# Optimization experiments

Hardware: AMD Instinct MI355X
Metric: run time of the kernel (lower is better)

## Reference

```python
import jax, jax.numpy as jnp
import numpy as np

B, IN, OUT = 2048, 64, 2048


def setup_inputs() -> dict:
    key = jax.random.key(0)
    k1, k2, k3 = jax.random.split(key, 3)
    x = jax.random.normal(k1, (B, IN), dtype=jnp.float32)
    # learned params (shapes per init: means [in, out], inv_std_dev [out, in, in])
    means = jax.random.uniform(k2, (IN, OUT), dtype=jnp.float32)
    # roughly like the inverse of a diagonal step matrix plus small noise
    inv_std_dev = (jax.random.normal(k3, (OUT, IN, IN), dtype=jnp.float32) * 0.05
                   + jnp.eye(IN, dtype=jnp.float32) * 0.5)
    return {"x": x, "means": means, "inv_std_dev": inv_std_dev}


def reference(x, means, inv_std_dev):
    # diff[b, o, i] = x[b, i] - means[i, o]   -> [B, OUT, IN]
    d = x[:, None, :] - means.T[None, :, :]
    # torch uses inv_std_dev.pow(2) (elementwise square), not a matrix square
    A = inv_std_dev * inv_std_dev  # [OUT, IN, IN]
    # per-neuron quadratic form: q[b, o] = d[b,o,:] @ A[o] @ d[b,o,:]
    q = jnp.einsum('boi,oij,boj->bo', d, A, d)
    return jnp.exp(-0.5 * q)  # [B, OUT]
```

## Files before the change

### kernel.cpp

```cpp
#include <hip/hip_runtime.h>
#include <hip/hip_bf16.h>

typedef __bf16 bf16x8 __attribute__((ext_vector_type(8)));
typedef float f32x4 __attribute__((ext_vector_type(4)));
typedef float f32x16 __attribute__((ext_vector_type(16)));

#define B_N 2048
#define O_N 2048
#define K_N 64

__device__ __forceinline__ void gld16(const void* g, void* l) {
    __builtin_amdgcn_global_load_lds(
        (const __attribute__((address_space(1))) void*)g,
        (__attribute__((address_space(3))) void*)l,
        16, 0, 0);
}

__global__ __launch_bounds__(256) void rbf_prep(
    const float* __restrict__ inv, const float* __restrict__ means,
    __bf16* __restrict__ Atp, __bf16* __restrict__ cPhi,
    __bf16* __restrict__ cPlo, float* __restrict__ kArr)
{
    __shared__ float s[64 * 65];
    __shared__ float mld[64];
    __shared__ float uw[128];
    const int o = blockIdx.x;
    const int t = threadIdx.x;
    const float4* src = (const float4*)(inv + (size_t)o * 4096);
#pragma unroll
    for (int k = 0; k < 4; ++k) {
        const int idx = k * 256 + t;
        const float4 v = src[idx];
        const int i = idx >> 4;
        const int j0 = (idx & 15) * 4;
        s[i * 65 + j0 + 0] = v.x * v.x;
        s[i * 65 + j0 + 1] = v.y * v.y;
        s[i * 65 + j0 + 2] = v.z * v.z;
        s[i * 65 + j0 + 3] = v.w * v.w;
    }
    if (t < 64) mld[t] = means[(size_t)t * O_N + o];
    __syncthreads();
    if (t < 64) {
        float u = 0.f;
#pragma unroll
        for (int i = 0; i < 64; ++i) u = fmaf(s[i * 65 + t], mld[i], u);
        uw[t] = u;
    } else if (t < 128) {
        const int j = t - 64;
        float w = 0.f;
#pragma unroll
        for (int i = 0; i < 64; ++i) w = fmaf(s[j * 65 + i], mld[i], w);
        uw[64 + j] = w;
    }
    __syncthreads();
    if (t < 64) {
        const float c = -(uw[t] + uw[64 + t]);
        const __bf16 hi = (__bf16)c;
        const __bf16 lo = (__bf16)(c - (float)hi);
        const size_t eidx = (size_t)(o >> 5) * 2048 + (size_t)(t >> 4) * 512
                          + (size_t)(o & 31) * 16 + (t & 15);
        cPhi[eidx] = hi;
        cPlo[eidx] = lo;
    }
    if (t == 0) {
        float kk = 0.f;
#pragma unroll
        for (int j = 0; j < 64; ++j) kk = fmaf(uw[j], mld[j], kk);
        kArr[o] = kk;
    }
#pragma unroll
    for (int r = 0; r < 2; ++r) {
        const int ch = r * 256 + t;
        const int ss = ch >> 7;
        const int j = (ch >> 1) & 63;
        const int hh = ch & 1;
        bf16x8 v;
#pragma unroll
        for (int e = 0; e < 8; ++e)
            v[e] = (__bf16)s[(16 * ss + 8 * hh + e) * 65 + j];
        *(bf16x8*)(Atp + (size_t)o * 4096 + (size_t)ch * 8) = v;
    }
}

__global__ __launch_bounds__(256, 4) void rbf_main(
    const float* __restrict__ x, const __bf16* __restrict__ Atp,
    const __bf16* __restrict__ cPhi, const __bf16* __restrict__ cPlo,
    const float* __restrict__ kArr, float* __restrict__ out)
{
    __shared__ __align__(16) __bf16 sA[2][4096];
    __shared__ __align__(16) float sLin[4][32][32];
    __shared__ float sK[32];

    const int tid = threadIdx.x;
    const int wave = tid >> 6;
    const int lane = tid & 63;
    const int b = lane & 31;
    const int h = lane >> 5;

    const int wg = (int)blockIdx.x;
    const int xcd = wg & 7;
    const int loc = wg >> 3;
    const int og = xcd * 8 + (loc >> 4);
    const int bg = loc & 15;
    const int oBase = og * 32;
    const int rowW = bg * 128 + wave * 32;

    const float* xr = x + (size_t)(rowW + b) * K_N;

    const f32x16 zz = {0.f,0.f,0.f,0.f,0.f,0.f,0.f,0.f,
                       0.f,0.f,0.f,0.f,0.f,0.f,0.f,0.f};

    bf16x8 xh[4];
    f32x4 xd[2][4];
    {
        bf16x8 xl[4];
#pragma unroll
        for (int ss = 0; ss < 4; ++ss) {
            const float* p = xr + ss * 16 + h * 8;
            bf16x8 vh, vl;
#pragma unroll
            for (int e = 0; e < 8; ++e) {
                const float v = p[e];
                const __bf16 hi = (__bf16)v;
                vh[e] = hi;
                vl[e] = (__bf16)(v - (float)hi);
            }
            xh[ss] = vh; xl[ss] = vl;
        }
#pragma unroll
        for (int mt = 0; mt < 2; ++mt)
#pragma unroll
            for (int rq = 0; rq < 4; ++rq)
                xd[mt][rq] = *(const f32x4*)(xr + mt * 32 + rq * 8 + h * 4);

        const __bf16* chp = cPhi + (size_t)og * 2048;
        const __bf16* clp = cPlo + (size_t)og * 2048;
        f32x16 lin = zz;
#pragma unroll
        for (int ss = 0; ss < 4; ++ss) {
            const bf16x8 fh = *(const bf16x8*)(chp + ss * 512 + b * 16 + h * 8);
            const bf16x8 fl = *(const bf16x8*)(clp + ss * 512 + b * 16 + h * 8);
            lin = __builtin_amdgcn_mfma_f32_32x32x16_bf16(fh, xh[ss], lin, 0, 0, 0);
            lin = __builtin_amdgcn_mfma_f32_32x32x16_bf16(fh, xl[ss], lin, 0, 0, 0);
            lin = __builtin_amdgcn_mfma_f32_32x32x16_bf16(fl, xh[ss], lin, 0, 0, 0);
        }
#pragma unroll
        for (int r = 0; r < 16; ++r)
            sLin[wave][(r & 3) + 8 * (r >> 2) + 4 * h][b] = lin[r];
    }
    if (tid < 32) sK[tid] = kArr[oBase + tid];

    const int L0 = tid * 16, L1 = 4096 + tid * 16;
    const int S0 = L0 ^ (((L0 >> 7) & 7) << 4);
    const int S1 = L1 ^ (((L1 >> 7) & 7) << 4);
    const char* gp = (const char*)(Atp + (size_t)oBase * 4096);
    gld16(gp + S0, (char*)&sA[0][0] + L0);
    gld16(gp + S1, (char*)&sA[0][0] + L1);

    const int off0 = (b * 32 + h * 16) ^ (((b >> 2) & 7) << 4);
    float* outp = out + (size_t)(rowW + b) * O_N + oBase;

    float q4[4];
#pragma unroll 4
    for (int i = 0; i < 32; ++i) {
        __syncthreads();
        if (i < 31) {
            const char* gn = gp + (size_t)(i + 1) * 8192;
            char* ld = (char*)&sA[(i + 1) & 1][0];
            gld16(gn + S0, ld + L0);
            gld16(gn + S1, ld + L1);
        }
        const char* bufp = (const char*)&sA[i & 1][0];

        __builtin_amdgcn_s_setprio(1);
        f32x16 a0 = zz, a1 = zz;
#pragma unroll
        for (int ss = 0; ss < 4; ++ss) {
            const char* base = bufp + ss * 2048;
            const bf16x8 f0 = *(const bf16x8*)(base + off0);
            const bf16x8 f1 = *(const bf16x8*)(base + 1024 + off0);
            a0 = __builtin_amdgcn_mfma_f32_32x32x16_bf16(f0, xh[ss], a0, 0, 0, 0);
            a1 = __builtin_amdgcn_mfma_f32_32x32x16_bf16(f1, xh[ss], a1, 0, 0, 0);
        }
        __builtin_amdgcn_s_setprio(0);

        float p0 = 0.f, p1 = 0.f, p2 = 0.f, p3 = 0.f;
#pragma unroll
        for (int e = 0; e < 4; ++e) {
            p0 = fmaf(a0[e],      xd[0][0][e], p0);
            p1 = fmaf(a0[4 + e],  xd[0][1][e], p1);
            p2 = fmaf(a0[8 + e],  xd[0][2][e], p2);
            p3 = fmaf(a0[12 + e], xd[0][3][e], p3);
            p0 = fmaf(a1[e],      xd[1][0][e], p0);
            p1 = fmaf(a1[4 + e],  xd[1][1][e], p1);
            p2 = fmaf(a1[8 + e],  xd[1][2][e], p2);
            p3 = fmaf(a1[12 + e], xd[1][3][e], p3);
        }
        float q = (p0 + p1) + (p2 + p3);
        q += __shfl_xor(q, 32, 64);
        q += sLin[wave][i][b] + sK[i];
        q4[i & 3] = exp2f(q * -0.72134752044448170368f);

        if ((i & 3) == 3 && h == ((i >> 2) & 1)) {
            const f32x4 v = {q4[0], q4[1], q4[2], q4[3]};
            *(f32x4*)(outp + (i - 3)) = v;
        }
    }
}

extern "C" void kernel_launch(void* const* d_in, const int* in_sizes, int n_in,
                              void* d_out, int out_size, void* d_ws, size_t ws_size,
                              hipStream_t stream)
{
    const float* x = (const float*)d_in[0];
    const float* means = (const float*)d_in[1];
    const float* inv = (const float*)d_in[2];
    float* out = (float*)d_out;

    char* w = (char*)d_ws;
    __bf16* Atp  = (__bf16*)w;
    __bf16* cPhi = (__bf16*)(w + (size_t)O_N * 4096 * 2);
    __bf16* cPlo = (__bf16*)(w + (size_t)O_N * 4096 * 2 + 262144);
    float*  kArr = (float*)(w + (size_t)O_N * 4096 * 2 + 524288);

    rbf_prep<<<dim3(O_N), dim3(256), 0, stream>>>(inv, means, Atp, cPhi, cPlo, kArr);
    rbf_main<<<dim3(1024), dim3(256), 0, stream>>>(x, Atp, cPhi, cPlo, kArr, out);

    (void)in_sizes; (void)n_in; (void)out_size; (void)ws_size;
}
```

Measured before the change: 63.65 us.

## Quad-buffer A tiles, halve barriers, keep linear term in registers

The main loop now uses four LDS buffers and loads two A tiles per barrier, so there is one __syncthreads for every two output neurons instead of one per neuron. The linear term plus constant is kept in registers, with kArr added into the MFMA result, rather than being staged through the sLin/sK shared arrays. The loop is fully unrolled through macros, the first MFMA starts from zero instead of a zeroed accumulator, and the final dot uses packed two-wide FMAs. The exp is computed only in the half-wave that stores. LDS use goes from about 16.5KB to 32KB per block, which could limit occupancy under launch_bounds(256,4), and code size grows.

```diff
diff --git a/kernel.cpp b/kernel.cpp
--- a/kernel.cpp
+++ b/kernel.cpp
@@ -2,6 +2,7 @@
 #include <hip/hip_bf16.h>
 
 typedef __bf16 bf16x8 __attribute__((ext_vector_type(8)));
+typedef float f32x2 __attribute__((ext_vector_type(2)));
 typedef float f32x4 __attribute__((ext_vector_type(4)));
 typedef float f32x16 __attribute__((ext_vector_type(16)));
 
@@ -87,9 +88,7 @@
     const __bf16* __restrict__ cPhi, const __bf16* __restrict__ cPlo,
     const float* __restrict__ kArr, float* __restrict__ out)
 {
-    __shared__ __align__(16) __bf16 sA[2][4096];
-    __shared__ __align__(16) float sLin[4][32][32];
-    __shared__ float sK[32];
+    __shared__ __align__(16) __bf16 sA[4][4096];
 
     const int tid = threadIdx.x;
     const int wave = tid >> 6;
@@ -112,6 +111,7 @@
 
     bf16x8 xh[4];
     f32x4 xd[2][4];
+    f32x16 lin;
     {
         bf16x8 xl[4];
 #pragma unroll
@@ -135,7 +135,7 @@
 
         const __bf16* chp = cPhi + (size_t)og * 2048;
         const __bf16* clp = cPlo + (size_t)og * 2048;
-        f32x16 lin = zz;
+        lin = zz;
 #pragma unroll
         for (int ss = 0; ss < 4; ++ss) {
             const bf16x8 fh = *(const bf16x8*)(chp + ss * 512 + b * 16 + h * 8);
@@ -146,9 +146,8 @@
         }
 #pragma unroll
         for (int r = 0; r < 16; ++r)
-            sLin[wave][(r & 3) + 8 * (r >> 2) + 4 * h][b] = lin[r];
-    }
-    if (tid < 32) sK[tid] = kArr[oBase + tid];
+            lin[r] += kArr[oBase + (r & 3) + 8 * (r >> 2) + 4 * h];
+    }
 
     const int L0 = tid * 16, L1 = 4096 + tid * 16;
     const int S0 = L0 ^ (((L0 >> 7) & 7) << 4);
@@ -156,56 +155,85 @@
     const char* gp = (const char*)(Atp + (size_t)oBase * 4096);
     gld16(gp + S0, (char*)&sA[0][0] + L0);
     gld16(gp + S1, (char*)&sA[0][0] + L1);
+    gld16(gp + 8192 + S0, (char*)&sA[1][0] + L0);
+    gld16(gp + 8192 + S1, (char*)&sA[1][0] + L1);
 
     const int off0 = (b * 32 + h * 16) ^ (((b >> 2) & 7) << 4);
     float* outp = out + (size_t)(rowW + b) * O_N + oBase;
-
     float q4[4];
-#pragma unroll 4
-    for (int i = 0; i < 32; ++i) {
-        __syncthreads();
-        if (i < 31) {
-            const char* gn = gp + (size_t)(i + 1) * 8192;
-            char* ld = (char*)&sA[(i + 1) & 1][0];
-            gld16(gn + S0, ld + L0);
-            gld16(gn + S1, ld + L1);
-        }
-        const char* bufp = (const char*)&sA[i & 1][0];
-
-        __builtin_amdgcn_s_setprio(1);
-        f32x16 a0 = zz, a1 = zz;
-#pragma unroll
-        for (int ss = 0; ss < 4; ++ss) {
-            const char* base = bufp + ss * 2048;
-            const bf16x8 f0 = *(const bf16x8*)(base + off0);
-            const bf16x8 f1 = *(const bf16x8*)(base + 1024 + off0);
-            a0 = __builtin_amdgcn_mfma_f32_32x32x16_bf16(f0, xh[ss], a0, 0, 0, 0);
-            a1 = __builtin_amdgcn_mfma_f32_32x32x16_bf16(f1, xh[ss], a1, 0, 0, 0);
-        }
-        __builtin_amdgcn_s_setprio(0);
-
-        float p0 = 0.f, p1 = 0.f, p2 = 0.f, p3 = 0.f;
-#pragma unroll
-        for (int e = 0; e < 4; ++e) {
-            p0 = fmaf(a0[e],      xd[0][0][e], p0);
-            p1 = fmaf(a0[4 + e],  xd[0][1][e], p1);
-            p2 = fmaf(a0[8 + e],  xd[0][2][e], p2);
-            p3 = fmaf(a0[12 + e], xd[0][3][e], p3);
-            p0 = fmaf(a1[e],      xd[1][0][e], p0);
-            p1 = fmaf(a1[4 + e],  xd[1][1][e], p1);
-            p2 = fmaf(a1[8 + e],  xd[1][2][e], p2);
-            p3 = fmaf(a1[12 + e], xd[1][3][e], p3);
-        }
-        float q = (p0 + p1) + (p2 + p3);
-        q += __shfl_xor(q, 32, 64);
-        q += sLin[wave][i][b] + sK[i];
-        q4[i & 3] = exp2f(q * -0.72134752044448170368f);
-
-        if ((i & 3) == 3 && h == ((i >> 2) & 1)) {
-            const f32x4 v = {q4[0], q4[1], q4[2], q4[3]};
-            *(f32x4*)(outp + (i - 3)) = v;
-        }
-    }
+
+#define RBF_COMPUTE(I) do {                                                   \
+    const char* bufp_ = (const char*)&sA[(I) & 3][0];                         \
+    __builtin_amdgcn_s_setprio(1);                                            \
+    f32x16 a0_, a1_;                                                          \
+    {                                                                         \
+        const bf16x8 f0_ = *(const bf16x8*)(bufp_ + off0);                    \
+        const bf16x8 f1_ = *(const bf16x8*)(bufp_ + 1024 + off0);             \
+        a0_ = __builtin_amdgcn_mfma_f32_32x32x16_bf16(f0_, xh[0], zz, 0, 0, 0); \
+        a1_ = __builtin_amdgcn_mfma_f32_32x32x16_bf16(f1_, xh[0], zz, 0, 0, 0); \
+    }                                                                         \
+    _Pragma("unroll")                                                         \
+    for (int ss = 1; ss < 4; ++ss) {                                          \
+        const char* base_ = bufp_ + ss * 2048;                                \
+        const bf16x8 f0_ = *(const bf16x8*)(base_ + off0);                    \
+        const bf16x8 f1_ = *(const bf16x8*)(base_ + 1024 + off0);             \
+        a0_ = __builtin_amdgcn_mfma_f32_32x32x16_bf16(f0_, xh[ss], a0_, 0, 0, 0); \
+        a1_ = __builtin_amdgcn_mfma_f32_32x32x16_bf16(f1_, xh[ss], a1_, 0, 0, 0); \
+    }                                                                         \
+    __builtin_amdgcn_s_setprio(0);                                            \
+    f32x2 P0_ = {0.f, 0.f}, P1_ = {0.f, 0.f};                                 \
+    _Pragma("unroll")                                                         \
+    for (int rg = 0; rg < 4; ++rg) {                                          \
+        f32x2 u_, v_;                                                         \
+        u_[0] = a0_[rg*4+0]; u_[1] = a0_[rg*4+1];                             \
+        v_[0] = xd[0][rg][0]; v_[1] = xd[0][rg][1];                           \
+        P0_ = __builtin_elementwise_fma(u_, v_, P0_);                         \
+        u_[0] = a0_[rg*4+2]; u_[1] = a0_[rg*4+3];                             \
+        v_[0] = xd[0][rg][2]; v_[1] = xd[0][rg][3];                           \
+        P1_ = __builtin_elementwise_fma(u_, v_, P1_);                         \
+        u_[0] = a1_[rg*4+0]; u_[1] = a1_[rg*4+1];                             \
+        v_[0] = xd[1][rg][0]; v_[1] = xd[1][rg][1];                           \
+        P0_ = __builtin_elementwise_fma(u_, v_, P0_);                         \
+        u_[0] = a1_[rg*4+2]; u_[1] = a1_[rg*4+3];                             \
+        v_[0] = xd[1][rg][2]; v_[1] = xd[1][rg][3];                           \
+        P1_ = __builtin_elementwise_fma(u_, v_, P1_);                         \
+    }                                                                         \
+    const f32x2 Ps_ = P0_ + P1_;                                              \
+    float q_ = Ps_[0] + Ps_[1];                                               \
+    q_ += __shfl_xor(q_, 32, 64);                                             \
+    if (h == (((I) >> 2) & 1)) {                                              \
+        q4[(I) & 3] = exp2f((q_ + lin[((I) & 3) + (((I) >> 3) << 2)])         \
+                            * -0.72134752044448170368f);                      \
+        if (((I) & 3) == 3) {                                                 \
+            const f32x4 v_ = {q4[0], q4[1], q4[2], q4[3]};                    \
+            *(f32x4*)(outp + ((I) - 3)) = v_;                                 \
+        }                                                                     \
+    }                                                                         \
+} while (0)
+
+#define RBF_PHASE(P) do {                                                     \
+    __syncthreads();                                                          \
+    if ((P) < 15) {                                                           \
+        const char* g2_ = gp + (size_t)(2 * (P) + 2) * 8192;                  \
+        char* d2_ = (char*)&sA[(2 * (P) + 2) & 3][0];                         \
+        gld16(g2_ + S0, d2_ + L0);                                            \
+        gld16(g2_ + S1, d2_ + L1);                                            \
+        const char* g3_ = gp + (size_t)(2 * (P) + 3) * 8192;                  \
+        char* d3_ = (char*)&sA[(2 * (P) + 3) & 3][0];                         \
+        gld16(g3_ + S0, d3_ + L0);                                            \
+        gld16(g3_ + S1, d3_ + L1);                                            \
+    }                                                                         \
+    RBF_COMPUTE(2 * (P));                                                     \
+    RBF_COMPUTE(2 * (P) + 1);                                                 \
+} while (0)
+
+    RBF_PHASE(0);  RBF_PHASE(1);  RBF_PHASE(2);  RBF_PHASE(3);
+    RBF_PHASE(4);  RBF_PHASE(5);  RBF_PHASE(6);  RBF_PHASE(7);
+    RBF_PHASE(8);  RBF_PHASE(9);  RBF_PHASE(10); RBF_PHASE(11);
+    RBF_PHASE(12); RBF_PHASE(13); RBF_PHASE(14); RBF_PHASE(15);
+
+#undef RBF_PHASE
+#undef RBF_COMPUTE
 }
 
 extern "C" void kernel_launch(void* const* d_in, const int* in_sizes, int n_in,
```

After: 60.65 us. 4.7% less time.

## Recast per-neuron quadratic form as single GEMM over symmetric quadratic features

Applied to the files above, without the earlier changes.

Each quadratic form is expanded into upper-triangle monomial features x_i*x_j (2080 terms) plus linear and constant terms. Symmetrised A coefficients, the linear coefficients (split hi/lo) and the constant are packed into one K=2304 bf16 row per output, and matching feature rows per batch element. One plain 64x64-tiled bf16 MFMA GEMM plus an exp epilogue then replaces the per-output matrix-vector products and the FMA reductions. This trades a larger K (2304 against roughly 64x64 per output) for a regular GEMM, and adds preprocessing that writes about 18 MB of workspace. Accuracy may suffer because the x_i*x_j products and symmetrised coefficients are rounded to bf16 with no hi/lo split.

```diff
diff --git a/kernel.cpp b/kernel.cpp
--- a/kernel.cpp
+++ b/kernel.cpp
@@ -2,12 +2,13 @@
 #include <hip/hip_bf16.h>
 
 typedef __bf16 bf16x8 __attribute__((ext_vector_type(8)));
-typedef float f32x4 __attribute__((ext_vector_type(4)));
 typedef float f32x16 __attribute__((ext_vector_type(16)));
 
 #define B_N 2048
 #define O_N 2048
-#define K_N 64
+#define K_TRI 2080
+#define K_TOT 2304
+#define K_STEPS 36
 
 __device__ __forceinline__ void gld16(const void* g, void* l) {
     __builtin_amdgcn_global_load_lds(
@@ -16,195 +17,187 @@
         16, 0, 0);
 }
 
-__global__ __launch_bounds__(256) void rbf_prep(
+__global__ __launch_bounds__(256) void rbf_prep2(
     const float* __restrict__ inv, const float* __restrict__ means,
-    __bf16* __restrict__ Atp, __bf16* __restrict__ cPhi,
-    __bf16* __restrict__ cPlo, float* __restrict__ kArr)
+    const float* __restrict__ x, __bf16* __restrict__ S, __bf16* __restrict__ P)
 {
     __shared__ float s[64 * 65];
     __shared__ float mld[64];
     __shared__ float uw[128];
-    const int o = blockIdx.x;
+    __shared__ unsigned short ptab[K_TRI];
+
     const int t = threadIdx.x;
-    const float4* src = (const float4*)(inv + (size_t)o * 4096);
-#pragma unroll
-    for (int k = 0; k < 4; ++k) {
-        const int idx = k * 256 + t;
-        const float4 v = src[idx];
-        const int i = idx >> 4;
-        const int j0 = (idx & 15) * 4;
-        s[i * 65 + j0 + 0] = v.x * v.x;
-        s[i * 65 + j0 + 1] = v.y * v.y;
-        s[i * 65 + j0 + 2] = v.z * v.z;
-        s[i * 65 + j0 + 3] = v.w * v.w;
-    }
-    if (t < 64) mld[t] = means[(size_t)t * O_N + o];
-    __syncthreads();
-    if (t < 64) {
-        float u = 0.f;
-#pragma unroll
-        for (int i = 0; i < 64; ++i) u = fmaf(s[i * 65 + t], mld[i], u);
-        uw[t] = u;
-    } else if (t < 128) {
-        const int j = t - 64;
-        float w = 0.f;
-#pragma unroll
-        for (int i = 0; i < 64; ++i) w = fmaf(s[j * 65 + i], mld[i], w);
-        uw[64 + j] = w;
-    }
-    __syncthreads();
-    if (t < 64) {
-        const float c = -(uw[t] + uw[64 + t]);
-        const __bf16 hi = (__bf16)c;
-        const __bf16 lo = (__bf16)(c - (float)hi);
-        const size_t eidx = (size_t)(o >> 5) * 2048 + (size_t)(t >> 4) * 512
-                          + (size_t)(o & 31) * 16 + (t & 15);
-        cPhi[eidx] = hi;
-        cPlo[eidx] = lo;
-    }
-    if (t == 0) {
-        float kk = 0.f;
-#pragma unroll
-        for (int j = 0; j < 64; ++j) kk = fmaf(uw[j], mld[j], kk);
-        kArr[o] = kk;
-    }
-#pragma unroll
-    for (int r = 0; r < 2; ++r) {
-        const int ch = r * 256 + t;
-        const int ss = ch >> 7;
-        const int j = (ch >> 1) & 63;
-        const int hh = ch & 1;
-        bf16x8 v;
-#pragma unroll
-        for (int e = 0; e < 8; ++e)
-            v[e] = (__bf16)s[(16 * ss + 8 * hh + e) * 65 + j];
-        *(bf16x8*)(Atp + (size_t)o * 4096 + (size_t)ch * 8) = v;
-    }
-}
-
-__global__ __launch_bounds__(256, 4) void rbf_main(
-    const float* __restrict__ x, const __bf16* __restrict__ Atp,
-    const __bf16* __restrict__ cPhi, const __bf16* __restrict__ cPlo,
-    const float* __restrict__ kArr, float* __restrict__ out)
+    {
+        int base = 0;
+#pragma unroll 1
+        for (int i = 0; i < 64; ++i) {
+            if (t < 64 - i) ptab[base + t] = (unsigned short)((i << 8) | (i + t));
+            base += 64 - i;
+        }
+    }
+
+    if ((int)blockIdx.x < O_N) {
+        const int o = blockIdx.x;
+        const float4* src = (const float4*)(inv + (size_t)o * 4096);
+#pragma unroll
+        for (int k = 0; k < 4; ++k) {
+            const int idx = k * 256 + t;
+            const float4 v = src[idx];
+            const int i = idx >> 4;
+            const int j0 = (idx & 15) * 4;
+            s[i * 65 + j0 + 0] = v.x * v.x;
+            s[i * 65 + j0 + 1] = v.y * v.y;
+            s[i * 65 + j0 + 2] = v.z * v.z;
+            s[i * 65 + j0 + 3] = v.w * v.w;
+        }
+        if (t < 64) mld[t] = means[(size_t)t * O_N + o];
+        __syncthreads();
+        if (t < 64) {
+            float u = 0.f;
+#pragma unroll
+            for (int i = 0; i < 64; ++i) u = fmaf(s[i * 65 + t], mld[i], u);
+            uw[t] = u;
+        } else if (t < 128) {
+            const int j = t - 64;
+            float w = 0.f;
+#pragma unroll
+            for (int i = 0; i < 64; ++i) w = fmaf(s[j * 65 + i], mld[i], w);
+            uw[64 + j] = w;
+        }
+        __syncthreads();
+        __bf16* Srow = S + (size_t)o * K_TOT;
+#pragma unroll 1
+        for (int p = t; p < K_TRI; p += 256) {
+            const int ij = ptab[p];
+            const int i = ij >> 8, j = ij & 255;
+            const float v = (i == j) ? s[i * 65 + i]
+                                     : (s[i * 65 + j] + s[j * 65 + i]);
+            Srow[p] = (__bf16)v;
+        }
+        if (t < 64) {
+            const float c = -(uw[t] + uw[64 + t]);
+            const __bf16 hi = (__bf16)c;
+            const __bf16 lo = (__bf16)(c - (float)hi);
+            Srow[K_TRI + t] = hi;
+            Srow[K_TRI + 64 + t] = hi;
+            Srow[K_TRI + 128 + t] = lo;
+        }
+        if (t == 0) {
+            float kk = 0.f;
+#pragma unroll
+            for (int j = 0; j < 64; ++j) kk = fmaf(uw[j], mld[j], kk);
+            const __bf16 khi = (__bf16)kk;
+            const __bf16 klo = (__bf16)(kk - (float)khi);
+            Srow[2272] = khi;
+            Srow[2273] = klo;
+        }
+        if (t < K_TOT - 2274) Srow[2274 + t] = (__bf16)0.f;
+    } else {
+        const int b = (int)blockIdx.x - O_N;
+        if (t < 64) mld[t] = x[(size_t)b * 64 + t];
+        __syncthreads();
+        __bf16* Prow = P + (size_t)b * K_TOT;
+#pragma unroll 1
+        for (int p = t; p < K_TRI; p += 256) {
+            const int ij = ptab[p];
+            Prow[p] = (__bf16)(mld[ij >> 8] * mld[ij & 255]);
+        }
+        if (t < 64) {
+            const float v = mld[t];
+            const __bf16 hi = (__bf16)v;
+            Prow[K_TRI + t] = hi;
+            Prow[K_TRI + 64 + t] = (__bf16)(v - (float)hi);
+            Prow[K_TRI + 128 + t] = hi;
+        }
+        if (t == 0) {
+            Prow[2272] = (__bf16)1.f;
+            Prow[2273] = (__bf16)1.f;
+        }
+        if (t < K_TOT - 2274) Prow[2274 + t] = (__bf16)0.f;
+    }
+}
+
+__global__ __launch_bounds__(256, 4) void rbf_gemm(
+    const __bf16* __restrict__ P, const __bf16* __restrict__ S,
+    float* __restrict__ out)
 {
-    __shared__ __align__(16) __bf16 sA[2][4096];
-    __shared__ __align__(16) float sLin[4][32][32];
-    __shared__ float sK[32];
+    __shared__ __align__(16) char sP[2][8192];
+    __shared__ __align__(16) char sS[2][8192];
 
     const int tid = threadIdx.x;
-    const int wave = tid >> 6;
     const int lane = tid & 63;
-    const int b = lane & 31;
+    const int w = tid >> 6;
+    const int wr = w >> 1, wc = w & 1;
+    const int cl = lane & 31;
     const int h = lane >> 5;
 
     const int wg = (int)blockIdx.x;
     const int xcd = wg & 7;
     const int loc = wg >> 3;
-    const int og = xcd * 8 + (loc >> 4);
-    const int bg = loc & 15;
-    const int oBase = og * 32;
-    const int rowW = bg * 128 + wave * 32;
-
-    const float* xr = x + (size_t)(rowW + b) * K_N;
+    const int ogl = loc & 3;
+    const int bg = loc >> 2;
+    const int oBase = (xcd * 4 + ogl) * 64;
+    const int bBase = bg * 64;
+
+    const int L0 = tid * 16, L1 = 4096 + tid * 16;
+    const int r0 = L0 >> 7, r1 = L1 >> 7;
+    const int c0 = (L0 & 127) ^ ((r0 & 7) << 4);
+    const int c1 = (L1 & 127) ^ ((r1 & 7) << 4);
+    const char* gP0 = (const char*)P + (size_t)(bBase + r0) * (K_TOT * 2) + c0;
+    const char* gP1 = (const char*)P + (size_t)(bBase + r1) * (K_TOT * 2) + c1;
+    const char* gS0 = (const char*)S + (size_t)(oBase + r0) * (K_TOT * 2) + c0;
+    const char* gS1 = (const char*)S + (size_t)(oBase + r1) * (K_TOT * 2) + c1;
+
+    const int arow = wr * 32 + cl;
+    const int brow = wc * 32 + cl;
+    const char* aPb = &sP[0][0] + arow * 128;
+    const char* aSb = &sS[0][0] + brow * 128;
+    const int mA = (arow & 7) << 4;
+    const int mB = (brow & 7) << 4;
+
+    gld16(gP0, &sP[0][0] + L0);
+    gld16(gP1, &sP[0][0] + L1);
+    gld16(gS0, &sS[0][0] + L0);
+    gld16(gS1, &sS[0][0] + L1);
 
     const f32x16 zz = {0.f,0.f,0.f,0.f,0.f,0.f,0.f,0.f,
                        0.f,0.f,0.f,0.f,0.f,0.f,0.f,0.f};
-
-    bf16x8 xh[4];
-    f32x4 xd[2][4];
-    {
-        bf16x8 xl[4];
-#pragma unroll
-        for (int ss = 0; ss < 4; ++ss) {
-            const float* p = xr + ss * 16 + h * 8;
-            bf16x8 vh, vl;
-#pragma unroll
-            for (int e = 0; e < 8; ++e) {
-                const float v = p[e];
-                const __bf16 hi = (__bf16)v;
-                vh[e] = hi;
-                vl[e] = (__bf16)(v - (float)hi);
-            }
-            xh[ss] = vh; xl[ss] = vl;
-        }
-#pragma unroll
-        for (int mt = 0; mt < 2; ++mt)
-#pragma unroll
-            for (int rq = 0; rq < 4; ++rq)
-                xd[mt][rq] = *(const f32x4*)(xr + mt * 32 + rq * 8 + h * 4);
-
-        const __bf16* chp = cPhi + (size_t)og * 2048;
-        const __bf16* clp = cPlo + (size_t)og * 2048;
-        f32x16 lin = zz;
-#pragma unroll
-        for (int ss = 0; ss < 4; ++ss) {
-            const bf16x8 fh = *(const bf16x8*)(chp + ss * 512 + b * 16 + h * 8);
-            const bf16x8 fl = *(const bf16x8*)(clp + ss * 512 + b * 16 + h * 8);
-            lin = __builtin_amdgcn_mfma_f32_32x32x16_bf16(fh, xh[ss], lin, 0, 0, 0);
-            lin = __builtin_amdgcn_mfma_f32_32x32x16_bf16(fh, xl[ss], lin, 0, 0, 0);
-            lin = __builtin_amdgcn_mfma_f32_32x32x16_bf16(fl, xh[ss], lin, 0, 0, 0);
-        }
-#pragma unroll
-        for (int r = 0; r < 16; ++r)
-            sLin[wave][(r & 3) + 8 * (r >> 2) + 4 * h][b] = lin[r];
-    }
-    if (tid < 32) sK[tid] = kArr[oBase + tid];
-
-    const int L0 = tid * 16, L1 = 4096 + tid * 16;
-    const int S0 = L0 ^ (((L0 >> 7) & 7) << 4);
-    const int S1 = L1 ^ (((L1 >> 7) & 7) << 4);
-    const char* gp = (const char*)(Atp + (size_t)oBase * 4096);
-    gld16(gp + S0, (char*)&sA[0][0] + L0);
-    gld16(gp + S1, (char*)&sA[0][0] + L1);
-
-    const int off0 = (b * 32 + h * 16) ^ (((b >> 2) & 7) << 4);
-    float* outp = out + (size_t)(rowW + b) * O_N + oBase;
-
-    float q4[4];
-#pragma unroll 4
-    for (int i = 0; i < 32; ++i) {
-        __syncthreads();
-        if (i < 31) {
-            const char* gn = gp + (size_t)(i + 1) * 8192;
-            char* ld = (char*)&sA[(i + 1) & 1][0];
-            gld16(gn + S0, ld + L0);
-            gld16(gn + S1, ld + L1);
-        }
-        const char* bufp = (const char*)&sA[i & 1][0];
-
+    f32x16 acc0 = zz, acc1 = zz;
+
+#pragma unroll 2
+    for (int st = 0; st < K_STEPS; ++st) {
+        __syncthreads();
+        if (st < K_STEPS - 1) {
+            const int nb = (st + 1) & 1;
+            const size_t go = (size_t)(st + 1) * 128;
+            gld16(gP0 + go, &sP[nb][0] + L0);
+            gld16(gP1 + go, &sP[nb][0] + L1);
+            gld16(gS0 + go, &sS[nb][0] + L0);
+            gld16(gS1 + go, &sS[nb][0] + L1);
+        }
+        const int bo = (st & 1) * 8192;
+        const bf16x8 a0 = *(const bf16x8*)(aPb + bo + ((0  + h * 16) ^ mA));
+        const bf16x8 b0 = *(const bf16x8*)(aSb + bo + ((0  + h * 16) ^ mB));
+        const bf16x8 a1 = *(const bf16x8*)(aPb + bo + ((32 + h * 16) ^ mA));
+        const bf16x8 b1 = *(const bf16x8*)(aSb + bo + ((32 + h * 16) ^ mB));
+        const bf16x8 a2 = *(const bf16x8*)(aPb + bo + ((64 + h * 16) ^ mA));
+        const bf16x8 b2 = *(const bf16x8*)(aSb + bo + ((64 + h * 16) ^ mB));
+        const bf16x8 a3 = *(const bf16x8*)(aPb + bo + ((96 + h * 16) ^ mA));
+        const bf16x8 b3 = *(const bf16x8*)(aSb + bo + ((96 + h * 16) ^ mB));
         __builtin_amdgcn_s_setprio(1);
-        f32x16 a0 = zz, a1 = zz;
-#pragma unroll
-        for (int ss = 0; ss < 4; ++ss) {
-            const char* base = bufp + ss * 2048;
-            const bf16x8 f0 = *(const bf16x8*)(base + off0);
-            const bf16x8 f1 = *(const bf16x8*)(base + 1024 + off0);
-            a0 = __builtin_amdgcn_mfma_f32_32x32x16_bf16(f0, xh[ss], a0, 0, 0, 0);
-            a1 = __builtin_amdgcn_mfma_f32_32x32x16_bf16(f1, xh[ss], a1, 0, 0, 0);
-        }
+        acc0 = __builtin_amdgcn_mfma_f32_32x32x16_bf16(a0, b0, acc0, 0, 0, 0);
+        acc1 = __builtin_amdgcn_mfma_f32_32x32x16_bf16(a1, b1, acc1, 0, 0, 0);
+        acc0 = __builtin_amdgcn_mfma_f32_32x32x16_bf16(a2, b2, acc0, 0, 0, 0);
+        acc1 = __builtin_amdgcn_mfma_f32_32x32x16_bf16(a3, b3, acc1, 0, 0, 0);
         __builtin_amdgcn_s_setprio(0);
-
-        float p0 = 0.f, p1 = 0.f, p2 = 0.f, p3 = 0.f;
-#pragma unroll
-        for (int e = 0; e < 4; ++e) {
-            p0 = fmaf(a0[e],      xd[0][0][e], p0);
-            p1 = fmaf(a0[4 + e],  xd[0][1][e], p1);
-            p2 = fmaf(a0[8 + e],  xd[0][2][e], p2);
-            p3 = fmaf(a0[12 + e], xd[0][3][e], p3);
-            p0 = fmaf(a1[e],      xd[1][0][e], p0);
-            p1 = fmaf(a1[4 + e],  xd[1][1][e], p1);
-            p2 = fmaf(a1[8 + e],  xd[1][2][e], p2);
-            p3 = fmaf(a1[12 + e], xd[1][3][e], p3);
-        }
-        float q = (p0 + p1) + (p2 + p3);
-        q += __shfl_xor(q, 32, 64);
-        q += sLin[wave][i][b] + sK[i];
-        q4[i & 3] = exp2f(q * -0.72134752044448170368f);
-
-        if ((i & 3) == 3 && h == ((i >> 2) & 1)) {
-            const f32x4 v = {q4[0], q4[1], q4[2], q4[3]};
-            *(f32x4*)(outp + (i - 3)) = v;
-        }
+    }
+
+    const f32x16 accv = acc0 + acc1;
+#pragma unroll
+    for (int r = 0; r < 16; ++r) {
+        const int row = (r & 3) + 8 * (r >> 2) + 4 * h;
+        out[(size_t)(bBase + wr * 32 + row) * O_N + oBase + wc * 32 + cl] =
+            exp2f(accv[r] * -0.72134752044448170368f);
     }
 }
 
@@ -217,14 +210,11 @@
     const float* inv = (const float*)d_in[2];
     float* out = (float*)d_out;
 
-    char* w = (char*)d_ws;
-    __bf16* Atp  = (__bf16*)w;
-    __bf16* cPhi = (__bf16*)(w + (size_t)O_N * 4096 * 2);
-    __bf16* cPlo = (__bf16*)(w + (size_t)O_N * 4096 * 2 + 262144);
-    float*  kArr = (float*)(w + (size_t)O_N * 4096 * 2 + 524288);
-
-    rbf_prep<<<dim3(O_N), dim3(256), 0, stream>>>(inv, means, Atp, cPhi, cPlo, kArr);
-    rbf_main<<<dim3(1024), dim3(256), 0, stream>>>(x, Atp, cPhi, cPlo, kArr, out);
+    __bf16* S = (__bf16*)d_ws;
+    __bf16* P = (__bf16*)((char*)d_ws + (size_t)O_N * K_TOT * sizeof(__bf16));
+
+    rbf_prep2<<<dim3(2 * O_N), dim3(256), 0, stream>>>(inv, means, x, S, P);
+    rbf_gemm<<<dim3(1024), dim3(256), 0, stream>>>(P, S, out);
 
     (void)in_sizes; (void)n_in; (void)out_size; (void)ws_size;
 }
```

New measurement: 60.79 us. -4.5%, faster.
